# Optimization experiments

Measured on AMD Instinct MI355X. Metric: run time of the kernel, lower is better.

The kernel has to match this reference:

```python
import jax, jax.numpy as jnp
from jax import lax
import numpy as np

EPS = 1e-5


def conv(x, w, b, stride=1, pad=0):
    y = lax.conv_general_dilated(x, w, (stride, stride), ((pad, pad), (pad, pad)),
                                 dimension_numbers=('NCHW', 'OIHW', 'NCHW'))
    return y + b[None, :, None, None]


def conv_t(x, w, b):
    # PyTorch ConvTranspose2d(k=3, s=2, p=1, output_padding=1): out = 2*H
    wt = jnp.flip(w, (2, 3)).transpose(1, 0, 2, 3)  # [out, in, kh, kw]
    y = lax.conv_general_dilated(x, wt, (1, 1), ((1, 2), (1, 2)),
                                 lhs_dilation=(2, 2),
                                 dimension_numbers=('NCHW', 'OIHW', 'NCHW'))
    return y + b[None, :, None, None]


def adalin(x, rho, gamma, beta):
    im = x.mean((2, 3), keepdims=True)
    iv = x.var((2, 3), keepdims=True)
    lm = x.mean((0, 2, 3), keepdims=True)
    lv = x.var((0, 2, 3), keepdims=True)
    mean = rho * im + (1.0 - rho) * lm
    var = rho * iv + (1.0 - rho) * lv
    return gamma * (x - mean) / jnp.sqrt(var + EPS) + beta


def inorm(x):
    return (x - x.mean((2, 3), keepdims=True)) / jnp.sqrt(x.var((2, 3), keepdims=True) + EPS)


def windowed_attention(feat, w_f, b_f, w_g, b_g, w_h, b_h, window=8):
    B, C, H, W = feat.shape
    stride = window // 2
    pad = window - stride
    f = conv(feat, w_f, b_f)
    g = conv(feat, w_g, b_g)
    h = conv(feat, w_h, b_h)
    Nh, Nw = H // stride, W // stride
    r = jnp.arange(window)
    hi = jnp.arange(Nh)[:, None] * stride + r  # [Nh, window], indices into padded rows
    wi = jnp.arange(Nw)[:, None] * stride + r  # [Nw, window]

    def windows(t):
        c = t.shape[1]
        tp = jnp.pad(t, ((0, 0), (0, 0), (0, pad), (0, pad)))
        tw = tp[:, :, hi, :][:, :, :, :, wi]
        return tw.transpose(0, 2, 4, 1, 3, 5).reshape(B, Nh, Nw, c, window * window)

    fw, gw, hw = windows(f), windows(g), windows(h)
    mask = ((hi < H)[:, None, :, None] & (wi < W)[None, :, None, :]).reshape(Nh, Nw, window * window)
    scores = jnp.einsum('bijcq,bijck->bijqk', fw, gw)  # [B, Nh, Nw, 64, 64]
    scores = jnp.where(mask[None, :, :, None, :], scores, jnp.float32(-1e30))
    att = jax.nn.softmax(scores, axis=-1)
    op = jnp.einsum('bijck,bijqk->bijcq', hw, att).reshape(B, Nh, Nw, C, window, window)
    # torch loop writes overlapping windows row-major into one buffer -> last write
    # its top-left stride x stride block.
    return op[:, :, :, :, :stride, :stride].transpose(0, 3, 1, 4, 2, 5).reshape(B, C, H, W)


def _forward(x, w_e1, b_e1, rho1, gam1, bet1, w_e2, b_e2, rho2, gam2, bet2,
             w_e3, b_e3, rho3, gam3, bet3, rw1, rb1, rw2, rb2,
             w_f, b_f, w_g, b_g, w_h, b_h,
             w_d1, b_d1, rho4, gam4, bet4, w_d2, b_d2, rho5, gam5, bet5,
             w_d3, b_d3):
    e = jax.nn.relu(adalin(conv(x, w_e1, b_e1, 1, 3), rho1, gam1, bet1))
    e = jax.nn.relu(adalin(conv(e, w_e2, b_e2, 2, 1), rho2, gam2, bet2))
    e = jax.nn.relu(adalin(conv(e, w_e3, b_e3, 2, 1), rho3, gam3, bet3))
    out = e
    for i in range(rw1.shape[0]):  # fixed small number of residual blocks
        res = out
        out = jax.nn.relu(inorm(conv(out, rw1[i], rb1[i], 1, 1)))
        out = inorm(conv(out, rw2[i], rb2[i], 1, 1))
        out = jax.nn.relu(out + res)
    attn = windowed_attention(out, w_f, b_f, w_g, b_g, w_h, b_h)
    d = jax.nn.relu(adalin(conv_t(out, w_d1, b_d1), rho4, gam4, bet4))
    d = jax.nn.relu(adalin(conv_t(d, w_d2, b_d2), rho5, gam5, bet5))
    img = jnp.tanh(conv(d, w_d3, b_d3, 1, 3))
    return img, attn


def setup_inputs() -> dict:
    key = jax.random.key(0)
    ks = iter(jax.random.split(key, 60))

    def rn(shape, s=0.05):
        return jax.random.normal(next(ks), shape, dtype=jnp.float32) * s

    def ru(shape):
        return jax.random.uniform(next(ks), shape, dtype=jnp.float32)

    ngf = 64
    inp = dict(
        x=jax.random.normal(next(ks), (4, 3, 512, 512), dtype=jnp.float32),
        w_e1=rn((ngf, 3, 7, 7)), b_e1=rn((ngf,)),
        rho1=ru((1, ngf, 1, 1)), gam1=1.0 + rn((1, ngf, 1, 1)), bet1=rn((1, ngf, 1, 1)),
        w_e2=rn((2 * ngf, ngf, 3, 3)), b_e2=rn((2 * ngf,)),
        rho2=ru((1, 2 * ngf, 1, 1)), gam2=1.0 + rn((1, 2 * ngf, 1, 1)), bet2=rn((1, 2 * ngf, 1, 1)),
        w_e3=rn((4 * ngf, 2 * ngf, 3, 3)), b_e3=rn((4 * ngf,)),
        rho3=ru((1, 4 * ngf, 1, 1)), gam3=1.0 + rn((1, 4 * ngf, 1, 1)), bet3=rn((1, 4 * ngf, 1, 1)),
        rw1=rn((4, 4 * ngf, 4 * ngf, 3, 3)), rb1=rn((4, 4 * ngf)),
        rw2=rn((4, 4 * ngf, 4 * ngf, 3, 3)), rb2=rn((4, 4 * ngf)),
        w_f=rn((ngf // 2, 4 * ngf, 1, 1)), b_f=rn((ngf // 2,)),
        w_g=rn((ngf // 2, 4 * ngf, 1, 1)), b_g=rn((ngf // 2,)),
        w_h=rn((4 * ngf, 4 * ngf, 1, 1)), b_h=rn((4 * ngf,)),
        w_d1=rn((4 * ngf, 2 * ngf, 3, 3)), b_d1=rn((2 * ngf,)),
        rho4=ru((1, 2 * ngf, 1, 1)), gam4=1.0 + rn((1, 2 * ngf, 1, 1)), bet4=rn((1, 2 * ngf, 1, 1)),
        w_d2=rn((2 * ngf, ngf, 3, 3)), b_d2=rn((ngf,)),
        rho5=ru((1, ngf, 1, 1)), gam5=1.0 + rn((1, ngf, 1, 1)), bet5=rn((1, ngf, 1, 1)),
        w_d3=rn((3, ngf, 7, 7)), b_d3=rn((3,)),
    )
    return inp


def reference(x, w_e1, b_e1, rho1, gam1, bet1, w_e2, b_e2, rho2, gam2, bet2,
              w_e3, b_e3, rho3, gam3, bet3, rw1, rb1, rw2, rb2,
              w_f, b_f, w_g, b_g, w_h, b_h,
              w_d1, b_d1, rho4, gam4, bet4, w_d2, b_d2, rho5, gam5, bet5,
              w_d3, b_d3):
    return _forward(x, w_e1, b_e1, rho1, gam1, bet1, w_e2, b_e2, rho2, gam2, bet2,
                    w_e3, b_e3, rho3, gam3, bet3, rw1, rb1, rw2, rb2,
                    w_f, b_f, w_g, b_g, w_h, b_h,
                    w_d1, b_d1, rho4, gam4, bet4, w_d2, b_d2, rho5, gam5, bet5,
                    w_d3, b_d3)
```

## Files before the change

### kernel.cpp

```cpp
#include <hip/hip_runtime.h>
#include <hip/hip_bf16.h>
#include <hip/hip_fp16.h>

#define EPSN 1e-5f

typedef __hip_bfloat16 bf16;
typedef __half f16;
typedef __attribute__((ext_vector_type(8))) short bf16x8;
typedef __attribute__((ext_vector_type(4))) float f32x4;

__device__ __forceinline__ float b2f(bf16 v) { return __bfloat162float(v); }
__device__ __forceinline__ bf16 f2b(float v) { return __float2bfloat16(v); }
__device__ __forceinline__ unsigned short f2bu(float v) {
  bf16 h = __float2bfloat16(v);
  return *reinterpret_cast<unsigned short*>(&h);
}
__device__ __forceinline__ float bu2f(unsigned short u) {
  unsigned int b = ((unsigned int)u) << 16;
  return __uint_as_float(b);
}
__device__ __forceinline__ unsigned short f2hu(float v) {
  f16 h = __float2half(v);
  return *reinterpret_cast<unsigned short*>(&h);
}
__device__ __forceinline__ float hu2f(unsigned short u) {
  f16 h = *reinterpret_cast<f16*>(&u);
  return __half2float(h);
}
__device__ __forceinline__ void stv(bf16* p, size_t i, float v) { p[i] = f2b(v); }
__device__ __forceinline__ void stv(float* p, size_t i, float v) { p[i] = v; }
__device__ __forceinline__ void stv(f16* p, size_t i, float v) {
  p[i] = __float2half(v);
}

__device__ __forceinline__ unsigned short xbits(float v) { return f2bu(v); }
__device__ __forceinline__ unsigned short xbits(bf16 v) {
  return *reinterpret_cast<unsigned short*>(&v);
}

__device__ __forceinline__ float4 ld4(const float* p) { return *(const float4*)p; }
__device__ __forceinline__ float4 ld4(const bf16* p) {
  ushort4 u = *(const ushort4*)p;
  float4 r;
  r.x = bu2f(u.x);
  r.y = bu2f(u.y);
  r.z = bu2f(u.z);
  r.w = bu2f(u.w);
  return r;
}
__device__ __forceinline__ void st4(float* p, float4 v) { *(float4*)p = v; }
__device__ __forceinline__ void st4(bf16* p, float4 v) {
  uint2 o;
  o.x = (unsigned)f2bu(v.x) | ((unsigned)f2bu(v.y) << 16);
  o.y = (unsigned)f2bu(v.z) | ((unsigned)f2bu(v.w) << 16);
  *(uint2*)p = o;
}

__global__ void zero_stats_kernel(float* __restrict__ stats) {
  for (int k = threadIdx.x; k < 2048; k += 256) stats[k] = 0.f;
}

__global__ __launch_bounds__(256) void convert_w_kernel(
    const float* __restrict__ rw1, const float* __restrict__ rw2,
    unsigned short* __restrict__ wb) {
  int i = blockIdx.x * 256 + threadIdx.x;
  if (i >= 4718592) return;
  int conv = i / 589824;
  int rem = i % 589824;
  int tap = rem / 65536;
  int cc = rem % 65536;
  const float* src = ((conv & 1) ? rw2 : rw1) + (size_t)(conv >> 1) * 589824;
  float v = src[(size_t)cc * 9 + tap];
  bf16 h = __float2bfloat16(v);
  float fh = __bfloat162float(h);
  wb[i] = *reinterpret_cast<unsigned short*>(&h);
  bf16 l = __float2bfloat16(v - fh);
  wb[4718592 + i] = *reinterpret_cast<unsigned short*>(&l);
}

__global__ __launch_bounds__(256) void convert_wd_kernel(
    const float* __restrict__ w, unsigned short* __restrict__ out, int Ci,
    int Co) {
  int i = blockIdx.x * 256 + threadIdx.x;
  int total = 9 * Co * Ci;
  if (i >= total) return;
  int tap = i / (Co * Ci);
  int rem = i % (Co * Ci);
  int co = rem / Ci;
  int ci = rem % Ci;
  out[i] = f2bu(w[((size_t)ci * Co + co) * 9 + tap]);
}

__global__ __launch_bounds__(256) void convert_ws2_kernel(
    const float* __restrict__ w, unsigned short* __restrict__ out, int Ci,
    int Co) {
  int i = blockIdx.x * 256 + threadIdx.x;
  int total = 9 * Co * Ci;
  if (i >= total) return;
  int tap = i / (Co * Ci);
  int rem = i % (Co * Ci);
  int co = rem / Ci;
  int ci = rem % Ci;
  float v = w[((size_t)co * Ci + ci) * 9 + tap];
  bf16 h = __float2bfloat16(v);
  float fh = __bfloat162float(h);
  out[i] = *reinterpret_cast<unsigned short*>(&h);
  bf16 l = __float2bfloat16(v - fh);
  out[total + i] = *reinterpret_cast<unsigned short*>(&l);
}

__device__ __forceinline__ int swz3(int idx) {
  return (idx & 3) ^ ((idx >> 2) & 1);
}

__global__ __launch_bounds__(256) void conv3x3s1_mfma(
    const float* __restrict__ x, const unsigned short* __restrict__ wh,
    const unsigned short* __restrict__ wl, const float* __restrict__ bias,
    float* __restrict__ y) {
  const int H = 128, W = 128;
  int r = blockIdx.x;
  int cog = blockIdx.y;
  int n = blockIdx.z;
  int tid = threadIdx.x;
  int wv = tid >> 6, lane = tid & 63;
  int wco = (wv >> 1) * 64, wpx = (wv & 1) * 64;
  int l15 = lane & 15, l4 = lane >> 4;

  __shared__ __align__(16) unsigned short Xh[3 * 130 * 32];
  __shared__ __align__(16) unsigned short Xl[3 * 130 * 32];
  __shared__ __align__(16) unsigned short Ah[128 * 32];
  __shared__ __align__(16) unsigned short Al[128 * 32];

  f32x4 acc[4][4];
#pragma unroll
  for (int m = 0; m < 4; ++m)
#pragma unroll
    for (int nf = 0; nf < 4; ++nf) acc[m][nf] = (f32x4){0.f, 0.f, 0.f, 0.f};

  const float* xn0 = x + (size_t)n * 256 * H * W;

  for (int cb = 0; cb < 8; ++cb) {
    int ci0 = cb * 32;
    {
      const float* xn = xn0 + (size_t)ci0 * H * W;
      for (int t = tid; t < 1560; t += 256) {
        int q = t & 3;
        int cr = t >> 2;
        int col = cr % 130;
        int row = cr / 130;
        int gr = r + row - 1;
        int gc = col - 1;
        bool ok = (gr >= 0) && (gr < H) && (gc >= 0) && (gc < W);
        uint4 ph = {0, 0, 0, 0};
        uint4 pl = {0, 0, 0, 0};
        if (ok) {
          const float* xp =
              xn + (size_t)(q * 8) * (H * W) + (size_t)gr * W + gc;
          unsigned short vh[8], vl[8];
#pragma unroll
          for (int e = 0; e < 8; ++e) {
            float v = xp[(size_t)e * H * W];
            bf16 hb = __float2bfloat16(v);
            float fh = __bfloat162float(hb);
            bf16 lb = __float2bfloat16(v - fh);
            vh[e] = *reinterpret_cast<unsigned short*>(&hb);
            vl[e] = *reinterpret_cast<unsigned short*>(&lb);
          }
          ph.x = (unsigned)vh[0] | ((unsigned)vh[1] << 16);
          ph.y = (unsigned)vh[2] | ((unsigned)vh[3] << 16);
          ph.z = (unsigned)vh[4] | ((unsigned)vh[5] << 16);
          ph.w = (unsigned)vh[6] | ((unsigned)vh[7] << 16);
          pl.x = (unsigned)vl[0] | ((unsigned)vl[1] << 16);
          pl.y = (unsigned)vl[2] | ((unsigned)vl[3] << 16);
          pl.z = (unsigned)vl[4] | ((unsigned)vl[5] << 16);
          pl.w = (unsigned)vl[6] | ((unsigned)vl[7] << 16);
        }
        int slot = (cr * 4 + (q ^ swz3(col))) * 8;
        *(uint4*)(&Xh[slot]) = ph;
        *(uint4*)(&Xl[slot]) = pl;
      }
    }
    for (int tap = 0; tap < 9; ++tap) {
      for (int t = tid; t < 1024; t += 256) {
        int half = t >> 9;
        int rem = t & 511;
        int q = rem & 3;
        int co = rem >> 2;
        const unsigned short* wsrc =
            (half ? wl : wh) +
            ((size_t)tap * 256 + cog * 128 + co) * 256 + ci0 + q * 8;
        uint4 pk = *(const uint4*)wsrc;
        int slot = (co * 4 + (q ^ swz3(co))) * 8;
        *(uint4*)((half ? Al : Ah) + slot) = pk;
      }
      __syncthreads();
      int ky = tap / 3;
      int kx = tap - ky * 3;
      bf16x8 ahf[4], alf[4], bhf[4], blf[4];
#pragma unroll
      for (int m = 0; m < 4; ++m) {
        int co = wco + m * 16 + l15;
        int slot = (co * 4 + (l4 ^ swz3(co))) * 8;
        ahf[m] = *(const bf16x8*)(&Ah[slot]);
        alf[m] = *(const bf16x8*)(&Al[slot]);
      }
#pragma unroll
      for (int nf = 0; nf < 4; ++nf) {
        int col = wpx + nf * 16 + l15 + kx;
        int slot = ((ky * 130 + col) * 4 + (l4 ^ swz3(col))) * 8;
        bhf[nf] = *(const bf16x8*)(&Xh[slot]);
        blf[nf] = *(const bf16x8*)(&Xl[slot]);
      }
#pragma unroll
      for (int m = 0; m < 4; ++m)
#pragma unroll
        for (int nf = 0; nf < 4; ++nf) {
          acc[m][nf] = __builtin_amdgcn_mfma_f32_16x16x32_bf16(
              ahf[m], bhf[nf], acc[m][nf], 0, 0, 0);
          acc[m][nf] = __builtin_amdgcn_mfma_f32_16x16x32_bf16(
              ahf[m], blf[nf], acc[m][nf], 0, 0, 0);
          acc[m][nf] = __builtin_amdgcn_mfma_f32_16x16x32_bf16(
              alf[m], bhf[nf], acc[m][nf], 0, 0, 0);
        }
      __syncthreads();
    }
  }
#pragma unroll
  for (int m = 0; m < 4; ++m) {
    int cob = cog * 128 + wco + m * 16 + l4 * 4;
#pragma unroll
    for (int reg = 0; reg < 4; ++reg) {
      float bv = bias[cob + reg];
      float* yr =
          y + (((size_t)(n * 256 + cob + reg) * H) + r) * W + wpx + l15;
#pragma unroll
      for (int nf = 0; nf < 4; ++nf) yr[nf * 16] = acc[m][nf][reg] + bv;
    }
  }
}

template <typename Tout>
__global__ __launch_bounds__(256) void conv3x3s2_mfma(
    const f16* __restrict__ x, const unsigned short* __restrict__ wch,
    const unsigned short* __restrict__ wcl, const float* __restrict__ bias,
    const float* __restrict__ stats, Tout* __restrict__ y, int Ci, int Hi,
    int Wi, int Cotot) {
  int Ho = Hi >> 1, Wo = Wi >> 1;
  int r = blockIdx.x;
  int npx = Wo >> 6;
  int pxg = blockIdx.y % npx;
  int cog = blockIdx.y / npx;
  int n = blockIdx.z;
  int tid = threadIdx.x;
  int wv = tid >> 6, lane = tid & 63;
  int wv_co = wv >> 1, wv_px = wv & 1;
  int l15 = lane & 15, l4 = lane >> 4;
  int pxbase = pxg * 64;

  __shared__ __align__(16) unsigned short Xeh[3 * 64 * 32];
  __shared__ __align__(16) unsigned short Xel[3 * 64 * 32];
  __shared__ __align__(16) unsigned short Xoh[3 * 68 * 32];
  __shared__ __align__(16) unsigned short Xol[3 * 68 * 32];
  __shared__ __align__(16) unsigned short Ah[128 * 32];
  __shared__ __align__(16) unsigned short Al[128 * 32];

  f32x4 acc[4][2];
#pragma unroll
  for (int m = 0; m < 4; ++m)
#pragma unroll
    for (int nf = 0; nf < 2; ++nf) acc[m][nf] = (f32x4){0.f, 0.f, 0.f, 0.f};

  const f16* xb = x + (size_t)n * Ci * Hi * Wi;
  int nchunk = Ci >> 5;
  for (int cb = 0; cb < nchunk; ++cb) {
    int ci0 = cb * 32;
    for (int t = tid; t < 1548; t += 256) {
      bool isodd = t >= 768;
      int tt = isodd ? (t - 768) : t;
      int q = tt & 3;
      int cr = tt >> 2;
      int i, idx;
      if (!isodd) {
        i = cr >> 6;
        idx = cr & 63;
      } else {
        i = cr / 65;
        idx = cr % 65;
      }
      int gr = 2 * r - 1 + i;
      int gc = isodd ? (2 * pxbase + 2 * idx - 1) : (2 * (pxbase + idx));
      uint4 ph = {0, 0, 0, 0};
      uint4 pl4 = {0, 0, 0, 0};
      if (gr >= 0 && gr < Hi && gc >= 0 && gc < Wi) {
        const f16* xp = xb + ((size_t)(ci0 + q * 8) * Hi + gr) * Wi + gc;
        const float* scp = stats + 2048 + n * Ci + ci0 + q * 8;
        const float* shp = stats + 3072 + n * Ci + ci0 + q * 8;
        unsigned short vh[8], vl[8];
#pragma unroll
        for (int e = 0; e < 8; ++e) {
          float raw = (float)xp[(size_t)e * Hi * Wi];
          float v = fmaxf(fmaf(raw, scp[e], shp[e]), 0.f);
          bf16 hb = __float2bfloat16(v);
          float fh = __bfloat162float(hb);
          bf16 lb = __float2bfloat16(v - fh);
          vh[e] = *reinterpret_cast<unsigned short*>(&hb);
          vl[e] = *reinterpret_cast<unsigned short*>(&lb);
        }
        ph.x = (unsigned)vh[0] | ((unsigned)vh[1] << 16);
        ph.y = (unsigned)vh[2] | ((unsigned)vh[3] << 16);
        ph.z = (unsigned)vh[4] | ((unsigned)vh[5] << 16);
        ph.w = (unsigned)vh[6] | ((unsigned)vh[7] << 16);
        pl4.x = (unsigned)vl[0] | ((unsigned)vl[1] << 16);
        pl4.y = (unsigned)vl[2] | ((unsigned)vl[3] << 16);
        pl4.z = (unsigned)vl[4] | ((unsigned)vl[5] << 16);
        pl4.w = (unsigned)vl[6] | ((unsigned)vl[7] << 16);
      }
      int stride = isodd ? 68 : 64;
      int slot = ((i * stride + idx) * 4 + (q ^ swz3(idx))) * 8;
      if (isodd) {
        *(uint4*)(&Xoh[slot]) = ph;
        *(uint4*)(&Xol[slot]) = pl4;
      } else {
        *(uint4*)(&Xeh[slot]) = ph;
        *(uint4*)(&Xel[slot]) = pl4;
      }
    }
#pragma unroll
    for (int tap = 0; tap < 9; ++tap) {
      const int ky = tap / 3, kx = tap % 3;
      for (int t = tid; t < 1024; t += 256) {
        int half = t >> 9;
        int rem = t & 511;
        int q = rem & 3;
        int co = rem >> 2;
        const unsigned short* wsrc =
            (half ? wcl : wch) +
            ((size_t)tap * Cotot + cog * 128 + co) * Ci + ci0 + q * 8;
        uint4 pk = *(const uint4*)wsrc;
        int slot = (co * 4 + (q ^ swz3(co))) * 8;
        *(uint4*)((half ? Al : Ah) + slot) = pk;
      }
      __syncthreads();
      bf16x8 ahf[4], alf[4], bhf[2], blf[2];
#pragma unroll
      for (int m = 0; m < 4; ++m) {
        int co = wv_co * 64 + m * 16 + l15;
        int slot = (co * 4 + (l4 ^ swz3(co))) * 8;
        ahf[m] = *(const bf16x8*)(&Ah[slot]);
        alf[m] = *(const bf16x8*)(&Al[slot]);
      }
#pragma unroll
      for (int nf = 0; nf < 2; ++nf) {
        int pl = wv_px * 32 + nf * 16 + l15;
        if (kx == 1) {
          int slot = ((ky * 64 + pl) * 4 + (l4 ^ swz3(pl))) * 8;
          bhf[nf] = *(const bf16x8*)(&Xeh[slot]);
          blf[nf] = *(const bf16x8*)(&Xel[slot]);
        } else {
          int idx = (kx == 0) ? pl : (pl + 1);
          int slot = ((ky * 68 + idx) * 4 + (l4 ^ swz3(idx))) * 8;
          bhf[nf] = *(const bf16x8*)(&Xoh[slot]);
          blf[nf] = *(const bf16x8*)(&Xol[slot]);
        }
      }
#pragma unroll
      for (int m = 0; m < 4; ++m)
#pragma unroll
        for (int nf = 0; nf < 2; ++nf) {
          acc[m][nf] = __builtin_amdgcn_mfma_f32_16x16x32_bf16(
              ahf[m], bhf[nf], acc[m][nf], 0, 0, 0);
          acc[m][nf] = __builtin_amdgcn_mfma_f32_16x16x32_bf16(
              ahf[m], blf[nf], acc[m][nf], 0, 0, 0);
          acc[m][nf] = __builtin_amdgcn_mfma_f32_16x16x32_bf16(
              alf[m], bhf[nf], acc[m][nf], 0, 0, 0);
        }
      __syncthreads();
    }
  }
#pragma unroll
  for (int m = 0; m < 4; ++m) {
#pragma unroll
    for (int reg = 0; reg < 4; ++reg) {
      int co = cog * 128 + wv_co * 64 + m * 16 + l4 * 4 + reg;
      float bv = bias[co];
#pragma unroll
      for (int nf = 0; nf < 2; ++nf) {
        int px = pxbase + wv_px * 32 + nf * 16 + l15;
        stv(y, ((size_t)(n * Cotot + co) * Ho + r) * Wo + px,
            acc[m][nf][reg] + bv);
      }
    }
  }
}

template <int MF, typename Tin>
__global__ __launch_bounds__(256) void convt3x3_mfma(
    const Tin* __restrict__ x, const unsigned short* __restrict__ wc,
    const float* __restrict__ bias, bf16* __restrict__ y, int Ci, int Hi,
    int Wi) {
  const int Co = MF * 32;
  int Ho = Hi * 2, Wo = Wi * 2;
  int r = blockIdx.x;
  int c0 = blockIdx.y * 64;
  int n = blockIdx.z;
  int tid = threadIdx.x;
  int wv = tid >> 6, lane = tid & 63;
  int wv_co = wv >> 1, wv_px = wv & 1;
  int l15 = lane & 15, l4 = lane >> 4;

  __shared__ __align__(16) unsigned short Xs[2 * 66 * 32];
  __shared__ __align__(16) unsigned short As[MF * 32 * 32 * 2];

  f32x4 acc[4][MF][2];
#pragma unroll
  for (int par = 0; par < 4; ++par)
#pragma unroll
    for (int m = 0; m < MF; ++m)
#pragma unroll
      for (int nf = 0; nf < 2; ++nf)
        acc[par][m][nf] = (f32x4){0.f, 0.f, 0.f, 0.f};

  const Tin* xb = x + (size_t)n * Ci * Hi * Wi;
  int nchunk = Ci >> 5;
  for (int cb = 0; cb < nchunk; ++cb) {
    int ci0 = cb * 32;
    for (int t = tid; t < 520; t += 256) {
      int q = t & 3;
      int cr = t >> 2;
      int col = cr % 65;
      int row = cr / 65;
      int gr = r + row;
      int gc = c0 + col;
      uint4 pk = {0, 0, 0, 0};
      if (gr < Hi && gc < Wi) {
        const Tin* xp = xb + ((size_t)(ci0 + q * 8) * Hi + gr) * Wi + gc;
        unsigned short v[8];
#pragma unroll
        for (int e = 0; e < 8; ++e) v[e] = xbits(xp[(size_t)e * Hi * Wi]);
        pk.x = (unsigned)v[0] | ((unsigned)v[1] << 16);
        pk.y = (unsigned)v[2] | ((unsigned)v[3] << 16);
        pk.z = (unsigned)v[4] | ((unsigned)v[5] << 16);
        pk.w = (unsigned)v[6] | ((unsigned)v[7] << 16);
      }
      int slot = ((row * 66 + col) * 4 + (q ^ swz3(col))) * 8;
      *(uint4*)(&Xs[slot]) = pk;
    }
#pragma unroll
    for (int tap = 0; tap < 9; ++tap) {
      const int ky = tap / 3, kx = tap % 3;
      const int par = ((ky != 1) ? 2 : 0) + ((kx != 1) ? 1 : 0);
      const int trow = (ky == 0) ? 1 : 0;
      const int tcol = (kx == 0) ? 1 : 0;
      for (int t = tid; t < Co * 4; t += 256) {
        int q = t & 3;
        int co = t >> 2;
        uint4 pk =
            *(const uint4*)(wc + ((size_t)tap * Co + co) * Ci + ci0 + q * 8);
        int slot = (co * 4 + (q ^ swz3(co))) * 8;
        *(uint4*)(&As[slot]) = pk;
      }
      __syncthreads();
      bf16x8 af[MF], bfr[2];
#pragma unroll
      for (int m = 0; m < MF; ++m) {
        int co = wv_co * (MF * 16) + m * 16 + l15;
        int slot = (co * 4 + (l4 ^ swz3(co))) * 8;
        af[m] = *(const bf16x8*)(&As[slot]);
      }
#pragma unroll
      for (int nf = 0; nf < 2; ++nf) {
        int lc = wv_px * 32 + nf * 16 + l15 + tcol;
        int slot = ((trow * 66 + lc) * 4 + (l4 ^ swz3(lc))) * 8;
        bfr[nf] = *(const bf16x8*)(&Xs[slot]);
      }
#pragma unroll
      for (int m = 0; m < MF; ++m)
#pragma unroll
        for (int nf = 0; nf < 2; ++nf)
          acc[par][m][nf] = __builtin_amdgcn_mfma_f32_16x16x32_bf16(
              af[m], bfr[nf], acc[par][m][nf], 0, 0, 0);
      __syncthreads();
    }
  }
#pragma unroll
  for (int par = 0; par < 4; ++par) {
    int py = par >> 1, pxp = par & 1;
    int orow = 2 * r + py;
#pragma unroll
    for (int m = 0; m < MF; ++m) {
#pragma unroll
      for (int reg = 0; reg < 4; ++reg) {
        int co = wv_co * (MF * 16) + m * 16 + l4 * 4 + reg;
        float bv = bias[co];
        bf16* yr = y + ((size_t)(n * Co + co) * Ho + orow) * Wo + pxp;
#pragma unroll
        for (int nf = 0; nf < 2; ++nf) {
          int px_in = c0 + wv_px * 32 + nf * 16 + l15;
          yr[2 * px_in] = f2b(acc[par][m][nf][reg] + bv);
        }
      }
    }
  }
}

__global__ __launch_bounds__(256) void conv7_e1(
    const float* __restrict__ x, const float* __restrict__ w,
    const float* __restrict__ bias, float* __restrict__ stats,
    f16* __restrict__ y) {
  const int H = 512, W = 512;
  __shared__ float Xs[5200];
  __shared__ float wsh[8 * 3 * 49];
  __shared__ float sred[4][8], qred[4][8];
  int cog = blockIdx.y;
  int n = blockIdx.z;
  int tid = threadIdx.x;
  int r0 = blockIdx.x * 4;
  int tr = tid >> 6;
  int lane = tid & 63;
  for (int t = tid; t < 1176; t += 256) wsh[t] = w[cog * 1176 + t];
  const float* xb = x + (size_t)n * 3 * H * W;
  float acc[8][8];
#pragma unroll
  for (int j = 0; j < 8; ++j) {
#pragma unroll
    for (int p = 0; p < 8; ++p) acc[j][p] = 0.f;
  }
  for (int ci = 0; ci < 3; ++ci) {
    __syncthreads();
    for (int t = tid; t < 5200; t += 256) {
      int row = t / 520;
      int col = t - row * 520;
      int gr = r0 - 3 + row;
      int gc = col - 3;
      float v = 0.f;
      if (gr >= 0 && gr < H && gc >= 0 && gc < W)
        v = xb[((size_t)ci * H + gr) * W + gc];
      Xs[t] = v;
    }
    __syncthreads();
    for (int i = 0; i < 7; ++i) {
      const float* xr = &Xs[(tr + i) * 520 + lane];
      float v[8][7];
#pragma unroll
      for (int p = 0; p < 8; ++p)
#pragma unroll
        for (int k = 0; k < 7; ++k) v[p][k] = xr[p * 64 + k];
#pragma unroll
      for (int j = 0; j < 8; ++j) {
        const float* wr = &wsh[(j * 3 + ci) * 49 + i * 7];
        float w0 = wr[0], w1 = wr[1], w2 = wr[2], w3 = wr[3], w4 = wr[4],
              w5 = wr[5], w6 = wr[6];
#pragma unroll
        for (int p = 0; p < 8; ++p)
          acc[j][p] += v[p][0] * w0 + v[p][1] * w1 + v[p][2] * w2 +
                       v[p][3] * w3 + v[p][4] * w4 + v[p][5] * w5 +
                       v[p][6] * w6;
      }
    }
  }
  int r = r0 + tr;
#pragma unroll
  for (int j = 0; j < 8; ++j) {
    int co = cog * 8 + j;
    float bv = bias[co];
    f16* yr = y + ((size_t)(n * 64 + co) * H + r) * W + lane;
    float s = 0.f, q = 0.f;
#pragma unroll
    for (int p = 0; p < 8; ++p) {
      float o = acc[j][p] + bv;
      yr[p * 64] = __float2half(o);
      s += o;
      q += o * o;
    }
#pragma unroll
    for (int off = 32; off > 0; off >>= 1) {
      s += __shfl_down(s, off, 64);
      q += __shfl_down(q, off, 64);
    }
    if (lane == 0) {
      sred[tr][j] = s;
      qred[tr][j] = q;
    }
  }
  __syncthreads();
  if (tid < 8) {
    float S = sred[0][tid] + sred[1][tid] + sred[2][tid] + sred[3][tid];
    float Q = qred[0][tid] + qred[1][tid] + qred[2][tid] + qred[3][tid];
    atomicAdd(&stats[n * 64 + cog * 8 + tid], S);
    atomicAdd(&stats[1024 + n * 64 + cog * 8 + tid], Q);
  }
}

__global__ __launch_bounds__(256) void conv7_head_mfma(
    const bf16* __restrict__ xin, const float* __restrict__ w,
    const float* __restrict__ bias, float* __restrict__ y) {
  const int H = 512, W = 512;
  __shared__ __align__(16) unsigned short Xs[10 * 264 * 8];
  __shared__ __align__(16) unsigned short wlds[7 * 16 * 64];
  int n = blockIdx.z;
  int cbase = blockIdx.y * 256;
  int r0 = blockIdx.x * 4;
  int tid = threadIdx.x;
  int wv = tid >> 6;
  int lane = tid & 63;
  int l15 = lane & 15, l4 = lane >> 4;
  const unsigned short* xb =
      (const unsigned short*)xin + (size_t)n * 64 * H * W;
  f32x4 acc[16];
#pragma unroll
  for (int nf = 0; nf < 16; ++nf) acc[nf] = (f32x4){0.f, 0.f, 0.f, 0.f};
  for (int ch = 0; ch < 8; ++ch) {
    __syncthreads();
    for (int t = tid; t < 2640; t += 256) {
      int row = t / 264;
      int col = t - row * 264;
      int gr = r0 - 3 + row;
      int gc = cbase - 3 + col;
      uint4 pk = {0, 0, 0, 0};
      if (gr >= 0 && gr < H && gc >= 0 && gc < W) {
        const unsigned short* xp =
            xb + ((size_t)(ch * 8) * H + gr) * W + gc;
        unsigned short v[8];
#pragma unroll
        for (int e = 0; e < 8; ++e) v[e] = xp[(size_t)e * H * W];
        pk.x = (unsigned)v[0] | ((unsigned)v[1] << 16);
        pk.y = (unsigned)v[2] | ((unsigned)v[3] << 16);
        pk.z = (unsigned)v[4] | ((unsigned)v[5] << 16);
        pk.w = (unsigned)v[6] | ((unsigned)v[7] << 16);
      }
      *(uint4*)(&Xs[t * 8]) = pk;
    }
    for (int t = tid; t < 7168; t += 256) {
      int k64 = t & 63;
      int co = (t >> 6) & 15;
      int ky = t >> 10;
      int kx = k64 >> 3;
      int cie = k64 & 7;
      unsigned short val = 0;
      if (co < 3 && kx < 7)
        val = f2bu(w[((size_t)(co * 64 + ch * 8 + cie) * 7 + ky) * 7 + kx]);
      wlds[t] = val;
    }
    __syncthreads();
#pragma unroll 1
    for (int ky = 0; ky < 7; ++ky) {
      bf16x8 af0 = *(const bf16x8*)(&wlds[(ky * 16 + l15) * 64 + l4 * 8]);
      bf16x8 af1 =
          *(const bf16x8*)(&wlds[(ky * 16 + l15) * 64 + 32 + l4 * 8]);
      int xrow = wv + ky;
#pragma unroll
      for (int nf = 0; nf < 16; ++nf) {
        int col0 = nf * 16 + l15 + l4;
        bf16x8 b0 = *(const bf16x8*)(&Xs[(xrow * 264 + col0) * 8]);
        acc[nf] =
            __builtin_amdgcn_mfma_f32_16x16x32_bf16(af0, b0, acc[nf], 0, 0, 0);
        bf16x8 b1 = *(const bf16x8*)(&Xs[(xrow * 264 + col0 + 4) * 8]);
        acc[nf] =
            __builtin_amdgcn_mfma_f32_16x16x32_bf16(af1, b1, acc[nf], 0, 0, 0);
      }
    }
  }
  if (l4 == 0) {
    int r = r0 + wv;
#pragma unroll
    for (int nf = 0; nf < 16; ++nf) {
#pragma unroll
      for (int reg = 0; reg < 3; ++reg) {
        float o = tanhf(acc[nf][reg] + bias[reg]);
        y[((size_t)(n * 3 + reg) * H + r) * W + cbase + nf * 16 + l15] = o;
      }
    }
  }
}

__global__ __launch_bounds__(256) void conv1x1_tile(
    const float* __restrict__ x, const float* __restrict__ w,
    const float* __restrict__ bias, float* __restrict__ y, int Ci, int HW) {
  int cog = blockIdx.y;
  int Co = gridDim.y * 4;
  int n = blockIdx.z;
  int p0 = (blockIdx.x * 256 + threadIdx.x) * 4;
  const float* xb = x + (size_t)n * Ci * HW + p0;
  float acc[4][4];
#pragma unroll
  for (int j = 0; j < 4; ++j) {
    float b = bias[cog * 4 + j];
#pragma unroll
    for (int p = 0; p < 4; ++p) acc[j][p] = b;
  }
  for (int ci = 0; ci < Ci; ++ci) {
    float4 xv = *(const float4*)(xb + (size_t)ci * HW);
#pragma unroll
    for (int j = 0; j < 4; ++j) {
      float wv = w[(size_t)(cog * 4 + j) * Ci + ci];
      acc[j][0] += xv.x * wv;
      acc[j][1] += xv.y * wv;
      acc[j][2] += xv.z * wv;
      acc[j][3] += xv.w * wv;
    }
  }
#pragma unroll
  for (int j = 0; j < 4; ++j) {
    float4 o = {acc[j][0], acc[j][1], acc[j][2], acc[j][3]};
    *(float4*)(y + (size_t)(n * Co + cog * 4 + j) * HW + p0) = o;
  }
}

template <typename Tin>
__global__ __launch_bounds__(256) void reduce_nc_kernel(
    const Tin* __restrict__ x, float* __restrict__ stats, int HW) {
  int b = blockIdx.x;
  const Tin* p = x + (size_t)b * HW;
  float s = 0.f, q = 0.f;
  for (int i = threadIdx.x; i < HW; i += 256) {
    float v = (float)p[i];
    s += v;
    q += v * v;
  }
  __shared__ float ss[256], qq[256];
  ss[threadIdx.x] = s;
  qq[threadIdx.x] = q;
  __syncthreads();
  for (int off = 128; off > 0; off >>= 1) {
    if (threadIdx.x < off) {
      ss[threadIdx.x] += ss[threadIdx.x + off];
      qq[threadIdx.x] += qq[threadIdx.x + off];
    }
    __syncthreads();
  }
  if (threadIdx.x == 0) {
    stats[b] = ss[0];
    stats[1024 + b] = qq[0];
  }
}

__global__ void adalin_coef_kernel(float* __restrict__ stats,
                                   const float* __restrict__ rho,
                                   const float* __restrict__ gam,
                                   const float* __restrict__ bet, int N, int C,
                                   float invHW) {
  int i = blockIdx.x * blockDim.x + threadIdx.x;
  if (i >= N * C) return;
  int c = i % C;
  const float* sums = stats;
  const float* sqs = stats + 1024;
  float im = sums[i] * invHW;
  float iv = sqs[i] * invHW - im * im;
  float lsum = 0.f, lsq = 0.f;
  for (int n = 0; n < N; ++n) {
    lsum += sums[n * C + c];
    lsq += sqs[n * C + c];
  }
  float lm = lsum * invHW / N;
  float lv = lsq * invHW / N - lm * lm;
  float r = rho[c];
  float mean = r * im + (1.f - r) * lm;
  float var = fmaxf(r * iv + (1.f - r) * lv, 0.f);
  float sc = gam[c] / sqrtf(var + EPSN);
  stats[2048 + i] = sc;
  stats[3072 + i] = bet[c] - mean * sc;
}

__global__ void inorm_coef_kernel(float* __restrict__ stats, int NC,
                                  float invHW) {
  int i = blockIdx.x * blockDim.x + threadIdx.x;
  if (i >= NC) return;
  float im = stats[i] * invHW;
  float iv = fmaxf(stats[1024 + i] * invHW - im * im, 0.f);
  float sc = 1.f / sqrtf(iv + EPSN);
  stats[2048 + i] = sc;
  stats[3072 + i] = -im * sc;
}

template <typename T>
__global__ __launch_bounds__(256) void scale_shift_kernel(
    T* __restrict__ x, const float* __restrict__ stats, int HW, size_t total,
    int relu) {
  size_t i = (size_t)blockIdx.x * 256 + threadIdx.x;
  if (i >= total) return;
  int nc = (int)(i / (size_t)HW);
  float v = (float)x[i] * stats[2048 + nc] + stats[3072 + nc];
  if (relu) v = fmaxf(v, 0.f);
  stv(x, i, v);
}

__global__ __launch_bounds__(256) void add_relu_kernel(
    float* __restrict__ dst, const float* __restrict__ a, size_t total) {
  size_t i = (size_t)blockIdx.x * 256 + threadIdx.x;
  if (i >= total) return;
  dst[i] = fmaxf(dst[i] + a[i], 0.f);
}

__global__ __launch_bounds__(256) void win_attn_kernel(
    const float* __restrict__ f, const float* __restrict__ g,
    const float* __restrict__ h, float* __restrict__ out) {
  const int H = 128;
  int j = blockIdx.x;
  int i = blockIdx.y;
  int b = blockIdx.z;
  __shared__ float fs[32 * 64];
  __shared__ float gs[32 * 64];
  __shared__ float att[16 * 64];
  int t = threadIdx.x;
  for (int idx = t; idx < 32 * 64; idx += 256) {
    int c = idx >> 6, k = idx & 63;
    int hr = i * 4 + (k >> 3), wc = j * 4 + (k & 7);
    float fv = 0.f, gv = 0.f;
    if (hr < H && wc < H) {
      size_t o = ((size_t)(b * 32 + c) * H + hr) * H + wc;
      fv = f[o];
      gv = g[o];
    }
    fs[idx] = fv;
    gs[idx] = gv;
  }
  __syncthreads();
  for (int idx = t; idx < 1024; idx += 256) {
    int q = idx >> 6, k = idx & 63;
    int qi = (q >> 2) * 8 + (q & 3);
    int hr = i * 4 + (k >> 3), wc = j * 4 + (k & 7);
    float s;
    if (hr < H && wc < H) {
      s = 0.f;
      for (int c = 0; c < 32; ++c) s += fs[c * 64 + qi] * gs[c * 64 + k];
    } else {
      s = -1e30f;
    }
    att[idx] = s;
  }
  __syncthreads();
  if (t < 16) {
    float m = -1e30f;
    for (int k = 0; k < 64; ++k) m = fmaxf(m, att[t * 64 + k]);
    float d = 0.f;
    for (int k = 0; k < 64; ++k) {
      float e = expf(att[t * 64 + k] - m);
      att[t * 64 + k] = e;
      d += e;
    }
    float inv = 1.f / d;
    for (int k = 0; k < 64; ++k) att[t * 64 + k] *= inv;
  }
  __syncthreads();
  int c = t;
  float accs[16];
  for (int q = 0; q < 16; ++q) accs[q] = 0.f;
  const float* hb = h + (size_t)(b * 256 + c) * H * H;
  for (int k = 0; k < 64; ++k) {
    int hr = i * 4 + (k >> 3), wc = j * 4 + (k & 7);
    if (hr >= H || wc >= H) continue;
    float hv = hb[hr * H + wc];
    for (int q = 0; q < 16; ++q) accs[q] += hv * att[q * 64 + k];
  }
  for (int q = 0; q < 16; ++q) {
    int oh = i * 4 + (q >> 2), ow = j * 4 + (q & 3);
    out[((size_t)(b * 256 + c) * H + oh) * H + ow] = accs[q];
  }
}

extern "C" void kernel_launch(void* const* d_in, const int* in_sizes, int n_in,
                              void* d_out, int out_size, void* d_ws,
                              size_t ws_size, hipStream_t stream) {
  const float* x = (const float*)d_in[0];
  const float* w_e1 = (const float*)d_in[1];
  const float* b_e1 = (const float*)d_in[2];
  const float* rho1 = (const float*)d_in[3];
  const float* gam1 = (const float*)d_in[4];
  const float* bet1 = (const float*)d_in[5];
  const float* w_e2 = (const float*)d_in[6];
  const float* b_e2 = (const float*)d_in[7];
  const float* rho2 = (const float*)d_in[8];
  const float* gam2 = (const float*)d_in[9];
  const float* bet2 = (const float*)d_in[10];
  const float* w_e3 = (const float*)d_in[11];
  const float* b_e3 = (const float*)d_in[12];
  const float* rho3 = (const float*)d_in[13];
  const float* gam3 = (const float*)d_in[14];
  const float* bet3 = (const float*)d_in[15];
  const float* rw1 = (const float*)d_in[16];
  const float* rb1 = (const float*)d_in[17];
  const float* rw2 = (const float*)d_in[18];
  const float* rb2 = (const float*)d_in[19];
  const float* w_f = (const float*)d_in[20];
  const float* b_f = (const float*)d_in[21];
  const float* w_g = (const float*)d_in[22];
  const float* b_g = (const float*)d_in[23];
  const float* w_h = (const float*)d_in[24];
  const float* b_h = (const float*)d_in[25];
  const float* w_d1 = (const float*)d_in[26];
  const float* b_d1 = (const float*)d_in[27];
  const float* rho4 = (const float*)d_in[28];
  const float* gam4 = (const float*)d_in[29];
  const float* bet4 = (const float*)d_in[30];
  const float* w_d2 = (const float*)d_in[31];
  const float* b_d2 = (const float*)d_in[32];
  const float* rho5 = (const float*)d_in[33];
  const float* gam5 = (const float*)d_in[34];
  const float* bet5 = (const float*)d_in[35];
  const float* w_d3 = (const float*)d_in[36];
  const float* b_d3 = (const float*)d_in[37];

  char* wsb = (char*)d_ws;
  f16* E1H = (f16*)wsb;
  float* Cc = (float*)wsb;
  float* D = (float*)(wsb + 67108864);
  float* E = (float*)(wsb + 134217728);
  float* F1 = (float*)(wsb + 67108864);
  float* F2 = (float*)(wsb + 75497472);
  f16* B2H = (f16*)(wsb + 134217728);
  bf16* Bb2 = (bf16*)(wsb + 134217728);
  bf16* A2 = (bf16*)wsb;

  float* out_img = (float*)d_out;
  float* out_attn = out_img + 3145728;
  float* stats = (float*)d_out;
  unsigned short* wbres = (unsigned short*)((char*)d_out + 12582912);
  unsigned short* wd1c = (unsigned short*)((char*)d_out + 1048576);
  unsigned short* wd2c = (unsigned short*)((char*)d_out + 2097152);
  unsigned short* we2c = (unsigned short*)((char*)d_out + 3145728);
  unsigned short* we3c = (unsigned short*)((char*)d_out + 4194304);

  dim3 blk(256);

  convert_w_kernel<<<18432, blk, 0, stream>>>(rw1, rw2, wbres);
  convert_wd_kernel<<<1152, blk, 0, stream>>>(w_d1, wd1c, 256, 128);
  convert_wd_kernel<<<288, blk, 0, stream>>>(w_d2, wd2c, 128, 64);
  convert_ws2_kernel<<<288, blk, 0, stream>>>(w_e2, we2c, 64, 128);
  convert_ws2_kernel<<<1152, blk, 0, stream>>>(w_e3, we3c, 128, 256);

  zero_stats_kernel<<<1, 256, 0, stream>>>(stats);
  conv7_e1<<<dim3(128, 8, 4), blk, 0, stream>>>(x, w_e1, b_e1, stats, E1H);
  adalin_coef_kernel<<<1, 256, 0, stream>>>(stats, rho1, gam1, bet1, 4, 64,
                                            1.f / 262144.f);
  conv3x3s2_mfma<f16><<<dim3(256, 4, 4), blk, 0, stream>>>(
      E1H, we2c, we2c + 73728, b_e2, stats, B2H, 64, 512, 512, 128);
  reduce_nc_kernel<f16><<<512, blk, 0, stream>>>(B2H, stats, 65536);
  adalin_coef_kernel<<<2, 256, 0, stream>>>(stats, rho2, gam2, bet2, 4, 128,
                                            1.f / 65536.f);
  conv3x3s2_mfma<float><<<dim3(128, 4, 4), blk, 0, stream>>>(
      B2H, we3c, we3c + 294912, b_e3, stats, Cc, 128, 256, 256, 256);
  reduce_nc_kernel<float><<<1024, blk, 0, stream>>>(Cc, stats, 16384);
  adalin_coef_kernel<<<4, 256, 0, stream>>>(stats, rho3, gam3, bet3, 4, 256,
                                            1.f / 16384.f);
  scale_shift_kernel<float><<<65536, blk, 0, stream>>>(Cc, stats, 16384,
                                                       (size_t)16777216, 1);
  for (int r = 0; r < 4; ++r) {
    const float* rb1p = rb1 + (size_t)r * 256;
    const float* rb2p = rb2 + (size_t)r * 256;
    const unsigned short* w1h = wbres + (size_t)(r * 2) * 589824;
    const unsigned short* w1l = w1h + 4718592;
    const unsigned short* w2h = wbres + (size_t)(r * 2 + 1) * 589824;
    const unsigned short* w2l = w2h + 4718592;
    conv3x3s1_mfma<<<dim3(128, 2, 4), blk, 0, stream>>>(Cc, w1h, w1l, rb1p, D);
    reduce_nc_kernel<float><<<1024, blk, 0, stream>>>(D, stats, 16384);
    inorm_coef_kernel<<<4, 256, 0, stream>>>(stats, 1024, 1.f / 16384.f);
    scale_shift_kernel<float><<<65536, blk, 0, stream>>>(D, stats, 16384,
                                                         (size_t)16777216, 1);
    conv3x3s1_mfma<<<dim3(128, 2, 4), blk, 0, stream>>>(D, w2h, w2l, rb2p, E);
    reduce_nc_kernel<float><<<1024, blk, 0, stream>>>(E, stats, 16384);
    inorm_coef_kernel<<<4, 256, 0, stream>>>(stats, 1024, 1.f / 16384.f);
    scale_shift_kernel<float><<<65536, blk, 0, stream>>>(E, stats, 16384,
                                                         (size_t)16777216, 0);
    add_relu_kernel<<<65536, blk, 0, stream>>>(Cc, E, (size_t)16777216);
  }
  conv1x1_tile<<<dim3(16, 8, 4), blk, 0, stream>>>(Cc, w_f, b_f, F1, 256,
                                                   16384);
  conv1x1_tile<<<dim3(16, 8, 4), blk, 0, stream>>>(Cc, w_g, b_g, F2, 256,
                                                   16384);
  conv1x1_tile<<<dim3(16, 64, 4), blk, 0, stream>>>(Cc, w_h, b_h, E, 256,
                                                    16384);
  win_attn_kernel<<<dim3(32, 32, 4), blk, 0, stream>>>(F1, F2, E, out_attn);
  convt3x3_mfma<4, float><<<dim3(128, 2, 4), blk, 0, stream>>>(
      Cc, wd1c, b_d1, Bb2, 256, 128, 128);
  reduce_nc_kernel<bf16><<<512, blk, 0, stream>>>(Bb2, stats, 65536);
  adalin_coef_kernel<<<2, 256, 0, stream>>>(stats, rho4, gam4, bet4, 4, 128,
                                            1.f / 65536.f);
  scale_shift_kernel<bf16><<<131072, blk, 0, stream>>>(Bb2, stats, 65536,
                                                       (size_t)33554432, 1);
  convt3x3_mfma<2, bf16><<<dim3(256, 4, 4), blk, 0, stream>>>(
      Bb2, wd2c, b_d2, A2, 128, 256, 256);
  reduce_nc_kernel<bf16><<<256, blk, 0, stream>>>(A2, stats, 262144);
  adalin_coef_kernel<<<1, 256, 0, stream>>>(stats, rho5, gam5, bet5, 4, 64,
                                            1.f / 262144.f);
  scale_shift_kernel<bf16><<<262144, blk, 0, stream>>>(A2, stats, 262144,
                                                       (size_t)67108864, 1);
  conv7_head_mfma<<<dim3(128, 2, 4), blk, 0, stream>>>(A2, w_d3, b_d3,
                                                       out_img);
}
```

Baseline: 5.975 ms.

## Fuse norm scale-shift and ReLU into consumer conv tile loads

The standalone scale_shift passes over D, Bb2 and A2 are removed. Their per-channel affine plus ReLU is applied while the following 3x3, transposed-conv and 7x7 head kernels load input tiles, using coefficients read from the stats buffer. The E normalization is merged into the residual add-ReLU kernel, and the per-channel reduce kernel now uses vectorized 16-byte loads. The trade-off is extra per-element FMA work and coefficient reads inside the conv load loops, plus a small stats copy into a now-unused workspace region before the head conv.

```diff
diff --git a/kernel.cpp b/kernel.cpp
--- a/kernel.cpp
+++ b/kernel.cpp
@@ -31,11 +31,6 @@
 __device__ __forceinline__ void stv(float* p, size_t i, float v) { p[i] = v; }
 __device__ __forceinline__ void stv(f16* p, size_t i, float v) {
   p[i] = __float2half(v);
-}
-
-__device__ __forceinline__ unsigned short xbits(float v) { return f2bu(v); }
-__device__ __forceinline__ unsigned short xbits(bf16 v) {
-  return *reinterpret_cast<unsigned short*>(&v);
 }
 
 __device__ __forceinline__ float4 ld4(const float* p) { return *(const float4*)p; }
@@ -58,6 +53,12 @@
 
 __global__ void zero_stats_kernel(float* __restrict__ stats) {
   for (int k = threadIdx.x; k < 2048; k += 256) stats[k] = 0.f;
+}
+
+__global__ void copy_stats_kernel(const float* __restrict__ src,
+                                  float* __restrict__ dst) {
+  int i = blockIdx.x * 256 + threadIdx.x;
+  if (i < 4096) dst[i] = src[i];
 }
 
 __global__ __launch_bounds__(256) void convert_w_kernel(
@@ -113,10 +114,11 @@
   return (idx & 3) ^ ((idx >> 2) & 1);
 }
 
+template <bool NORM>
 __global__ __launch_bounds__(256) void conv3x3s1_mfma(
     const float* __restrict__ x, const unsigned short* __restrict__ wh,
     const unsigned short* __restrict__ wl, const float* __restrict__ bias,
-    float* __restrict__ y) {
+    const float* __restrict__ stats, float* __restrict__ y) {
   const int H = 128, W = 128;
   int r = blockIdx.x;
   int cog = blockIdx.y;
@@ -156,10 +158,13 @@
         if (ok) {
           const float* xp =
               xn + (size_t)(q * 8) * (H * W) + (size_t)gr * W + gc;
+          const float* scp = stats + 2048 + n * 256 + ci0 + q * 8;
+          const float* shp = stats + 3072 + n * 256 + ci0 + q * 8;
           unsigned short vh[8], vl[8];
 #pragma unroll
           for (int e = 0; e < 8; ++e) {
             float v = xp[(size_t)e * H * W];
+            if (NORM) v = fmaxf(fmaf(v, scp[e], shp[e]), 0.f);
             bf16 hb = __float2bfloat16(v);
             float fh = __bfloat162float(hb);
             bf16 lb = __float2bfloat16(v - fh);
@@ -393,11 +398,11 @@
   }
 }
 
-template <int MF, typename Tin>
+template <int MF, typename Tin, bool NORM>
 __global__ __launch_bounds__(256) void convt3x3_mfma(
     const Tin* __restrict__ x, const unsigned short* __restrict__ wc,
-    const float* __restrict__ bias, bf16* __restrict__ y, int Ci, int Hi,
-    int Wi) {
+    const float* __restrict__ bias, const float* __restrict__ stats,
+    bf16* __restrict__ y, int Ci, int Hi, int Wi) {
   const int Co = MF * 32;
   int Ho = Hi * 2, Wo = Wi * 2;
   int r = blockIdx.x;
@@ -434,9 +439,15 @@
       uint4 pk = {0, 0, 0, 0};
       if (gr < Hi && gc < Wi) {
         const Tin* xp = xb + ((size_t)(ci0 + q * 8) * Hi + gr) * Wi + gc;
+        const float* scp = stats + 2048 + n * Ci + ci0 + q * 8;
+        const float* shp = stats + 3072 + n * Ci + ci0 + q * 8;
         unsigned short v[8];
 #pragma unroll
-        for (int e = 0; e < 8; ++e) v[e] = xbits(xp[(size_t)e * Hi * Wi]);
+        for (int e = 0; e < 8; ++e) {
+          float raw = (float)xp[(size_t)e * Hi * Wi];
+          if (NORM) raw = fmaxf(fmaf(raw, scp[e], shp[e]), 0.f);
+          v[e] = f2bu(raw);
+        }
         pk.x = (unsigned)v[0] | ((unsigned)v[1] << 16);
         pk.y = (unsigned)v[2] | ((unsigned)v[3] << 16);
         pk.z = (unsigned)v[4] | ((unsigned)v[5] << 16);
@@ -593,7 +604,8 @@
 
 __global__ __launch_bounds__(256) void conv7_head_mfma(
     const bf16* __restrict__ xin, const float* __restrict__ w,
-    const float* __restrict__ bias, float* __restrict__ y) {
+    const float* __restrict__ bias, const float* __restrict__ stats,
+    float* __restrict__ y) {
   const int H = 512, W = 512;
   __shared__ __align__(16) unsigned short Xs[10 * 264 * 8];
   __shared__ __align__(16) unsigned short wlds[7 * 16 * 64];
@@ -620,9 +632,15 @@
       if (gr >= 0 && gr < H && gc >= 0 && gc < W) {
         const unsigned short* xp =
             xb + ((size_t)(ch * 8) * H + gr) * W + gc;
+        const float* scp = stats + 2048 + n * 64 + ch * 8;
+        const float* shp = stats + 3072 + n * 64 + ch * 8;
         unsigned short v[8];
 #pragma unroll
-        for (int e = 0; e < 8; ++e) v[e] = xp[(size_t)e * H * W];
+        for (int e = 0; e < 8; ++e) {
+          float raw = bu2f(xp[(size_t)e * H * W]);
+          raw = fmaxf(fmaf(raw, scp[e], shp[e]), 0.f);
+          v[e] = f2bu(raw);
+        }
         pk.x = (unsigned)v[0] | ((unsigned)v[1] << 16);
         pk.y = (unsigned)v[2] | ((unsigned)v[3] << 16);
         pk.z = (unsigned)v[4] | ((unsigned)v[5] << 16);
@@ -712,10 +730,31 @@
   int b = blockIdx.x;
   const Tin* p = x + (size_t)b * HW;
   float s = 0.f, q = 0.f;
-  for (int i = threadIdx.x; i < HW; i += 256) {
-    float v = (float)p[i];
-    s += v;
-    q += v * v;
+  if constexpr (sizeof(Tin) == 2) {
+    const uint4* p8 = reinterpret_cast<const uint4*>(p);
+    int n8 = HW >> 3;
+    for (int i = threadIdx.x; i < n8; i += 256) {
+      uint4 u = p8[i];
+      unsigned int wds[4] = {u.x, u.y, u.z, u.w};
+#pragma unroll
+      for (int j = 0; j < 4; ++j) {
+        unsigned short lo = (unsigned short)(wds[j] & 0xffff);
+        unsigned short hi = (unsigned short)(wds[j] >> 16);
+        Tin a = *reinterpret_cast<Tin*>(&lo);
+        Tin c = *reinterpret_cast<Tin*>(&hi);
+        float va = (float)a, vc = (float)c;
+        s += va + vc;
+        q += va * va + vc * vc;
+      }
+    }
+  } else {
+    const float4* p4 = reinterpret_cast<const float4*>(p);
+    int n4 = HW >> 2;
+    for (int i = threadIdx.x; i < n4; i += 256) {
+      float4 v = p4[i];
+      s += v.x + v.y + v.z + v.w;
+      q += v.x * v.x + v.y * v.y + v.z * v.z + v.w * v.w;
+    }
   }
   __shared__ float ss[256], qq[256];
   ss[threadIdx.x] = s;
@@ -784,11 +823,14 @@
   stv(x, i, v);
 }
 
-__global__ __launch_bounds__(256) void add_relu_kernel(
-    float* __restrict__ dst, const float* __restrict__ a, size_t total) {
+__global__ __launch_bounds__(256) void scale_add_relu_kernel(
+    float* __restrict__ dst, const float* __restrict__ e,
+    const float* __restrict__ stats, int HW, size_t total) {
   size_t i = (size_t)blockIdx.x * 256 + threadIdx.x;
   if (i >= total) return;
-  dst[i] = fmaxf(dst[i] + a[i], 0.f);
+  int nc = (int)(i / (size_t)HW);
+  float v = fmaf(e[i], stats[2048 + nc], stats[3072 + nc]);
+  dst[i] = fmaxf(dst[i] + v, 0.f);
 }
 
 __global__ __launch_bounds__(256) void win_attn_kernel(
@@ -910,6 +952,7 @@
   f16* B2H = (f16*)(wsb + 134217728);
   bf16* Bb2 = (bf16*)(wsb + 134217728);
   bf16* A2 = (bf16*)wsb;
+  float* statcopy = (float*)(wsb + 134217728);
 
   float* out_img = (float*)d_out;
   float* out_attn = out_img + 3145728;
@@ -951,17 +994,16 @@
     const unsigned short* w1l = w1h + 4718592;
     const unsigned short* w2h = wbres + (size_t)(r * 2 + 1) * 589824;
     const unsigned short* w2l = w2h + 4718592;
-    conv3x3s1_mfma<<<dim3(128, 2, 4), blk, 0, stream>>>(Cc, w1h, w1l, rb1p, D);
+    conv3x3s1_mfma<false><<<dim3(128, 2, 4), blk, 0, stream>>>(
+        Cc, w1h, w1l, rb1p, nullptr, D);
     reduce_nc_kernel<float><<<1024, blk, 0, stream>>>(D, stats, 16384);
     inorm_coef_kernel<<<4, 256, 0, stream>>>(stats, 1024, 1.f / 16384.f);
-    scale_shift_kernel<float><<<65536, blk, 0, stream>>>(D, stats, 16384,
-                                                         (size_t)16777216, 1);
-    conv3x3s1_mfma<<<dim3(128, 2, 4), blk, 0, stream>>>(D, w2h, w2l, rb2p, E);
+    conv3x3s1_mfma<true><<<dim3(128, 2, 4), blk, 0, stream>>>(
+        D, w2h, w2l, rb2p, stats, E);
     reduce_nc_kernel<float><<<1024, blk, 0, stream>>>(E, stats, 16384);
     inorm_coef_kernel<<<4, 256, 0, stream>>>(stats, 1024, 1.f / 16384.f);
-    scale_shift_kernel<float><<<65536, blk, 0, stream>>>(E, stats, 16384,
-                                                         (size_t)16777216, 0);
-    add_relu_kernel<<<65536, blk, 0, stream>>>(Cc, E, (size_t)16777216);
+    scale_add_relu_kernel<<<65536, blk, 0, stream>>>(Cc, E, stats, 16384,
+                                                     (size_t)16777216);
   }
   conv1x1_tile<<<dim3(16, 8, 4), blk, 0, stream>>>(Cc, w_f, b_f, F1, 256,
                                                    16384);
@@ -970,20 +1012,17 @@
   conv1x1_tile<<<dim3(16, 64, 4), blk, 0, stream>>>(Cc, w_h, b_h, E, 256,
                                                     16384);
   win_attn_kernel<<<dim3(32, 32, 4), blk, 0, stream>>>(F1, F2, E, out_attn);
-  convt3x3_mfma<4, float><<<dim3(128, 2, 4), blk, 0, stream>>>(
-      Cc, wd1c, b_d1, Bb2, 256, 128, 128);
+  convt3x3_mfma<4, float, false><<<dim3(128, 2, 4), blk, 0, stream>>>(
+      Cc, wd1c, b_d1, nullptr, Bb2, 256, 128, 128);
   reduce_nc_kernel<bf16><<<512, blk, 0, stream>>>(Bb2, stats, 65536);
   adalin_coef_kernel<<<2, 256, 0, stream>>>(stats, rho4, gam4, bet4, 4, 128,
                                             1.f / 65536.f);
-  scale_shift_kernel<bf16><<<131072, blk, 0, stream>>>(Bb2, stats, 65536,
-                                                       (size_t)33554432, 1);
-  convt3x3_mfma<2, bf16><<<dim3(256, 4, 4), blk, 0, stream>>>(
-      Bb2, wd2c, b_d2, A2, 128, 256, 256);
+  convt3x3_mfma<2, bf16, true><<<dim3(256, 4, 4), blk, 0, stream>>>(
+      Bb2, wd2c, b_d2, stats, A2, 128, 256, 256);
   reduce_nc_kernel<bf16><<<256, blk, 0, stream>>>(A2, stats, 262144);
   adalin_coef_kernel<<<1, 256, 0, stream>>>(stats, rho5, gam5, bet5, 4, 64,
                                             1.f / 262144.f);
-  scale_shift_kernel<bf16><<<262144, blk, 0, stream>>>(A2, stats, 262144,
-                                                       (size_t)67108864, 1);
+  copy_stats_kernel<<<16, blk, 0, stream>>>(stats, statcopy);
   conv7_head_mfma<<<dim3(128, 2, 4), blk, 0, stream>>>(A2, w_d3, b_d3,
-                                                       out_img);
-}
+                                                       statcopy, out_img);
+}
```

New measurement: 5.317 ms. -11.0%, faster.
